# Kernel optimization log

Hardware: AMD Instinct MI355X
Metric: run time of the kernel (lower is better)

Reference implementation:

```python
import jax, jax.numpy as jnp
import numpy as np

B, S, D, CH = 4, 2048, 1024, 64
MEM_LR, MEM_MOM, MEM_DECAY = 0.1, 0.9, 0.01
EPS = 1.1920929e-07  # torch RMSNorm default eps (float32 finfo eps)


def setup_inputs() -> dict:
    key = jax.random.key(0)
    ks = jax.random.split(key, 20)
    rn = lambda i, shape, s: jax.random.normal(ks[i], shape, dtype=jnp.float32) * s
    inp = {
        "x": jax.random.normal(ks[0], (B, S, D), dtype=jnp.float32),
        # archetypal metric M = I + small perturbation (near-identity, as in ArchetypalProjection)
        "Mmet": jnp.eye(D, dtype=jnp.float32)[None, :, :] + rn(1, (B, D, D), 0.02),
        # projections (bias-free, xavier-ish scale)
        "Wk": rn(2, (D, D), 0.02), "Wv": rn(3, (D, D), 0.02),
        "Wq": rn(4, (D, D), 0.02), "Wo": rn(5, (D, D), 0.02),
        # gate Linears (with bias) for decay / lr / momentum
        "Wgd": rn(6, (D, D), 0.02), "bgd": rn(7, (D,), 0.02),
        "Wgl": rn(8, (D, D), 0.02), "bgl": rn(9, (D,), 0.02),
        "Wgm": rn(10, (D, D), 0.02), "bgm": rn(11, (D,), 0.02),
        # RMSNorm gains
        "g_store": jnp.ones((D,), dtype=jnp.float32),
        "g_retr": jnp.ones((D,), dtype=jnp.float32),
        # memory MLP initial weights (depth=2, std=0.02)
        "W0": rn(12, (D, D), 0.02), "W1": rn(13, (D, D), 0.02),
    }
    return inp


def rmsnorm(x, g):
    return x * jax.lax.rsqrt(jnp.mean(x * x, axis=-1, keepdims=True) + EPS) * g


def l2norm(x):
    n = jnp.linalg.norm(x, axis=-1, keepdims=True)
    return x / jnp.maximum(n, 1e-12)


def mem_fwd(h, W0, W1):
    # 2-layer bias-free MLP with SiLU between layers (MemoryMLP, depth=2)
    return jax.nn.silu(h @ W0.T) @ W1.T


def forward(x, Mmet, Wk, Wv, Wq, Wo, Wgd, bgd, Wgl, bgl, Wgm, bgm, g_store, g_retr, W0, W1):
    Bs, Ss, Ds = x.shape
    pad = (-Ss) % CH
    xp = jnp.pad(x, ((0, 0), (0, pad), (0, 0))) if pad else x
    N = xp.shape[1] // CH

    # data-dependent per-chunk gates from chunk means -> batch-averaged scalars [N]
    cm = xp.reshape(Bs, N, CH, Ds).mean(axis=2)            # [B,N,D]
    alpha = jax.nn.sigmoid(cm @ Wgd.T + bgd).mean(-1).mean(0) * MEM_DECAY  # [N]
    theta = jax.nn.sigmoid(cm @ Wgl.T + bgl).mean(-1).mean(0) * MEM_LR     # [N]
    eta = jax.nn.sigmoid(cm @ Wgm.T + bgm).mean(-1).mean(0) * MEM_MOM      # [N]

    # store path: RMSNorm -> curved-space keys via archetypal metric
    xs = rmsnorm(xp, g_store)
    k = l2norm(jax.nn.silu(jnp.einsum('bsd,bde->bse', xs, Mmet) @ Wk.T))
    v = jax.nn.silu(xs @ Wv.T)
    # retrieve path
    q = l2norm(jax.nn.silu(rmsnorm(xp, g_retr) @ Wq.T))

    to_chunks = lambda t: t.reshape(Bs, N, CH, Ds).transpose(1, 0, 2, 3)  # [N,B,C,D]
    kc, vc, qc = to_chunks(k), to_chunks(v), to_chunks(q)

    def assoc_loss(params, kk, vv):
        return jnp.mean((mem_fwd(kk, *params) - vv) ** 2)

    grad_fn = jax.grad(assoc_loss)

    def step(carry, inp):
        W0c, W1c, S0, S1 = carry
        qt, kt, vt, a, th, et = inp
        r = mem_fwd(qt, W0c, W1c)                 # retrieve BEFORE update (causal)
        g0, g1 = grad_fn((W0c, W1c), kt, vt)      # surprise gradient
        S0n = et * S0 - th * g0                   # Eq. 14
        S1n = et * S1 - th * g1
        W0n = (1.0 - a) * W0c + S0n               # Eq. 13
        W1n = (1.0 - a) * W1c + S1n
        return (W0n, W1n, S0n, S1n), r

    init = (W0, W1, jnp.zeros_like(W0), jnp.zeros_like(W1))
    _, ret = jax.lax.scan(step, init, (qc, kc, vc, alpha, theta, eta))  # ret: [N,B,C,D]
    out = ret.transpose(1, 0, 2, 3).reshape(Bs, N * CH, Ds)[:, :Ss, :] @ Wo.T
    return out


def reference(x, Mmet, Wk, Wv, Wq, Wo, Wgd, bgd, Wgl, bgl, Wgm, bgm, g_store, g_retr, W0, W1):
    return forward(x, Mmet, Wk, Wv, Wq, Wo, Wgd, bgd, Wgl, bgl, Wgm, bgm, g_store, g_retr, W0, W1)
```

## Files before the change

### kernel.cpp

```cpp
#include <hip/hip_runtime.h>
#include <math.h>

static constexpr int B_ = 4, S_ = 2048, D_ = 1024, CH_ = 64, N_ = 32;
static constexpr float EPS_ = 1.1920929e-07f;
static constexpr float C2_  = 2.0f / 262144.0f;
static constexpr int GRID_ = 128;

typedef __attribute__((ext_vector_type(8))) short bf16x8;
typedef __attribute__((ext_vector_type(4))) short bf16x4;
typedef __attribute__((ext_vector_type(4))) float f32x4;

__device__ __forceinline__ float sigf(float x)  { return 1.f/(1.f+expf(-x)); }
__device__ __forceinline__ float siluf(float x) { return x/(1.f+expf(-x)); }
__device__ __forceinline__ float silugrad(float x){
  float s = 1.f/(1.f+expf(-x));
  return s*(1.f + x*(1.f-s));
}
__device__ __forceinline__ short f2b(float f){
  union{float f;unsigned u;}c; c.f=f;
  unsigned u=c.u;
  return (short)((u + 0x7fffu + ((u>>16)&1u)) >> 16);
}
__device__ __forceinline__ float b2f(short h){
  union{unsigned u;float f;}c; c.u=((unsigned)(unsigned short)h)<<16; return c.f;
}

template<int LPS>
__device__ __forceinline__ void wait_vm(int c){
  if (c <= 0)      asm volatile("s_waitcnt vmcnt(0)" ::: "memory");
  else if (c == 1) asm volatile("s_waitcnt vmcnt(%0)" :: "i"(LPS)   : "memory");
  else             asm volatile("s_waitcnt vmcnt(%0)" :: "i"(2*LPS) : "memory");
}

template<int MT, int NT, int DEPTH>
__device__ __forceinline__ void score(
    const short* __restrict__ A, const short* __restrict__ Bm,
    int K, int lda, int ldb, int bm0, int bn0, short* stg,
    f32x4 (&acc)[MT/32][NT/32])
{
  constexpr int MF = MT/32, NF = NT/32;
  constexpr int ACH = MT*8, BCH = NT*8, T = 256;
  constexpr int BUF = (MT+NT)*64;
  constexpr int LPS = (ACH+BCH)/T;
  const int tid = threadIdx.x, lane = tid & 63, w = tid >> 6;
  const int wm = w>>1, wn = w&1, lrow = lane & 15, lk8 = lane >> 4;

  #pragma unroll
  for (int i=0;i<MF;++i)
    #pragma unroll
    for (int j=0;j<NF;++j) acc[i][j] = (f32x4){0.f,0.f,0.f,0.f};

  auto stage = [&](int s){
    short* la = stg + (s & (DEPTH-1))*BUF;
    short* lb = la + MT*64;
    const int k0 = s*64;
    #pragma unroll
    for (int i=tid; i<ACH; i+=T){
      int row = i>>3, sc = (i&7) ^ (row&7);
      const short* src = A + (size_t)(bm0+row)*lda + k0 + (sc<<3);
      __builtin_amdgcn_global_load_lds(
        (const __attribute__((address_space(1))) void*)src,
        (__attribute__((address_space(3))) void*)(la + i*8), 16, 0, 0);
    }
    #pragma unroll
    for (int i=tid; i<BCH; i+=T){
      int row = i>>3, sc = (i&7) ^ (row&7);
      const short* src = Bm + (size_t)(bn0+row)*ldb + k0 + (sc<<3);
      __builtin_amdgcn_global_load_lds(
        (const __attribute__((address_space(1))) void*)src,
        (__attribute__((address_space(3))) void*)(lb + i*8), 16, 0, 0);
    }
  };

  const int nk = K >> 6;
  for (int s=0; s<DEPTH-1 && s<nk; ++s) stage(s);
  for (int ks=0; ks<nk; ++ks){
    int C = nk - ks; if (C > DEPTH-1) C = DEPTH-1;
    wait_vm<LPS>(C-1);
    __builtin_amdgcn_s_barrier();
    __builtin_amdgcn_sched_barrier(0);
    if (ks + DEPTH-1 < nk) stage(ks + DEPTH-1);
    short* la = stg + (ks & (DEPTH-1))*BUF;
    short* lb = la + MT*64;
    #pragma unroll
    for (int kk=0; kk<2; ++kk){
      bf16x8 af[MF], bfr[NF];
      #pragma unroll
      for (int mi=0;mi<MF;++mi){
        int row = wm*(MT/2) + mi*16 + lrow;
        int ch = row*8 + ((kk*4+lk8) ^ (row&7));
        af[mi] = *(const bf16x8*)(la + ch*8);
      }
      #pragma unroll
      for (int ni=0;ni<NF;++ni){
        int row = wn*(NT/2) + ni*16 + lrow;
        int ch = row*8 + ((kk*4+lk8) ^ (row&7));
        bfr[ni] = *(const bf16x8*)(lb + ch*8);
      }
      #pragma unroll
      for (int mi=0;mi<MF;++mi)
        #pragma unroll
        for (int ni=0;ni<NF;++ni)
          acc[mi][ni] = __builtin_amdgcn_mfma_f32_16x16x32_bf16(af[mi], bfr[ni], acc[mi][ni], 0,0,0);
    }
  }
}

template<int WMW, int WNW, int DEPTH, class Epi>
__device__ __forceinline__ void gemm_core(
    const short* __restrict__ A, const short* __restrict__ Bm,
    int K, int lda, int ldb, int bm0, int bn0, short* lds, Epi epi)
{
  constexpr int BK = 64, CPR = 8;
  constexpr int BMR = WMW*64, BNR = WNW*64, T = WMW*WNW*64;
  constexpr int ACH = BMR*CPR, BCH = BNR*CPR;
  constexpr int BUF = (BMR+BNR)*BK;
  constexpr int LPS = (ACH+BCH)/T;
  const int tid = threadIdx.x, lane = tid & 63, w = tid >> 6;
  const int wm = w / WNW, wn = w % WNW, lrow = lane & 15, lk8 = lane >> 4;

  f32x4 acc[4][4];
  #pragma unroll
  for (int i=0;i<4;++i)
    #pragma unroll
    for (int j=0;j<4;++j) acc[i][j] = (f32x4){0.f,0.f,0.f,0.f};

  auto stage = [&](int s){
    short* la = lds + (s & (DEPTH-1))*BUF;
    short* lb = la + BMR*BK;
    const int k0 = s*BK;
    #pragma unroll
    for (int i=tid; i<ACH; i+=T){
      int row = i>>3, sc = (i&7) ^ (row&7);
      const short* src = A + (size_t)(bm0+row)*lda + k0 + (sc<<3);
      __builtin_amdgcn_global_load_lds(
        (const __attribute__((address_space(1))) void*)src,
        (__attribute__((address_space(3))) void*)(la + i*8), 16, 0, 0);
    }
    #pragma unroll
    for (int i=tid; i<BCH; i+=T){
      int row = i>>3, sc = (i&7) ^ (row&7);
      const short* src = Bm + (size_t)(bn0+row)*ldb + k0 + (sc<<3);
      __builtin_amdgcn_global_load_lds(
        (const __attribute__((address_space(1))) void*)src,
        (__attribute__((address_space(3))) void*)(lb + i*8), 16, 0, 0);
    }
  };

  const int nk = K >> 6;
  for (int s=0; s<DEPTH-1 && s<nk; ++s) stage(s);
  for (int ks=0; ks<nk; ++ks){
    int C = nk - ks; if (C > DEPTH-1) C = DEPTH-1;
    wait_vm<LPS>(C-1);
    __builtin_amdgcn_s_barrier();
    __builtin_amdgcn_sched_barrier(0);
    if (ks + DEPTH-1 < nk) stage(ks + DEPTH-1);
    short* la = lds + (ks & (DEPTH-1))*BUF;
    short* lb = la + BMR*BK;
    #pragma unroll
    for (int kk=0; kk<2; ++kk){
      bf16x8 af[4], bfr[4];
      #pragma unroll
      for (int mi=0;mi<4;++mi){
        int row = wm*64 + mi*16 + lrow;
        int ch = row*8 + ((kk*4+lk8) ^ (row&7));
        af[mi] = *(const bf16x8*)(la + ch*8);
      }
      #pragma unroll
      for (int ni=0;ni<4;++ni){
        int row = wn*64 + ni*16 + lrow;
        int ch = row*8 + ((kk*4+lk8) ^ (row&7));
        bfr[ni] = *(const bf16x8*)(lb + ch*8);
      }
      #pragma unroll
      for (int mi=0;mi<4;++mi)
        #pragma unroll
        for (int ni=0;ni<4;++ni)
          acc[mi][ni] = __builtin_amdgcn_mfma_f32_16x16x32_bf16(af[mi], bfr[ni], acc[mi][ni], 0,0,0);
    }
  }
  #pragma unroll
  for (int mi=0;mi<4;++mi)
    #pragma unroll
    for (int ni=0;ni<4;++ni)
      epi(bm0 + wm*64 + mi*16 + lk8*4, bn0 + wn*64 + ni*16 + lrow, acc[mi][ni]);
}

struct EpiOut { float* C;
  __device__ void operator()(int r0,int c,f32x4 q) const {
    #pragma unroll
    for (int j=0;j<4;++j) C[(size_t)(r0+j)*D_+c]=q[j]; } };

struct EpiStoreBf { short* C;
  __device__ void operator()(int r0,int c,f32x4 q) const {
    #pragma unroll
    for (int j=0;j<4;++j) C[(size_t)(r0+j)*D_+c]=f2b(q[j]); } };

struct EpiBiasSig { float* C; const float* bias;
  __device__ void operator()(int r0,int c,f32x4 q) const {
    #pragma unroll
    for (int j=0;j<4;++j) C[(size_t)(r0+j)*D_+c] = sigf(q[j] + bias[c]); } };

struct EpiScat { short* dst; int part;
  __device__ void operator()(int r0,int c,f32x4 q) const {
    #pragma unroll
    for (int j=0;j<4;++j){
      int r = r0+j;
      int b = r >> 11, s = r & 2047, t = s >> 6, ch = s & 63;
      short sv = f2b(siluf(q[j]));
      if (part < 0) dst[((size_t)t*256 +             b*64 + ch)*D_ + c] = sv;
      else          dst[((size_t)t*512 + part*256 + b*64 + ch)*D_ + c] = sv;
    } } };

template<int WMW, int WNW, class Epi>
__global__ __launch_bounds__(WMW*WNW*64)
void mgemm(const short* __restrict__ A, const short* __restrict__ Bm,
           int K, int lda, int ldb, Epi epi){
  __shared__ __align__(16) short lds[2*(WMW+WNW)*64*64];
  gemm_core<WMW,WNW,2>(A, Bm, K, lda, ldb, blockIdx.y*WMW*64, blockIdx.x*WNW*64, lds, epi);
}

__device__ __forceinline__ void gsync(int* flags, int ep, bool do_rel, bool do_acq){
  asm volatile("s_waitcnt vmcnt(0) lgkmcnt(0)" ::: "memory");
  __syncthreads();
  const int bid = blockIdx.x, tid = threadIdx.x;
  int* rel = flags + 2048;
  if (tid == 0){
    if (do_rel) __builtin_amdgcn_fence(__ATOMIC_RELEASE, "agent");
    __hip_atomic_store(&flags[bid*16], ep, __ATOMIC_RELAXED, __HIP_MEMORY_SCOPE_SYSTEM);
  }
  if (bid == 0){
    if (tid < 64){
      for(;;){
        int a = __hip_atomic_load(&flags[tid*16],      __ATOMIC_RELAXED, __HIP_MEMORY_SCOPE_SYSTEM);
        int b = __hip_atomic_load(&flags[(tid+64)*16], __ATOMIC_RELAXED, __HIP_MEMORY_SCOPE_SYSTEM);
        if (__all(a >= ep && b >= ep)) break;
        __builtin_amdgcn_s_sleep(1);
      }
    }
    __syncthreads();
    if (tid == 0)
      __hip_atomic_store(rel, ep, __ATOMIC_RELAXED, __HIP_MEMORY_SCOPE_SYSTEM);
  }
  if (tid == 0){
    if (bid != 0)
      while (__hip_atomic_load(rel, __ATOMIC_RELAXED, __HIP_MEMORY_SCOPE_SYSTEM) < ep)
        __builtin_amdgcn_s_sleep(1);
    if (do_acq) __builtin_amdgcn_fence(__ATOMIC_ACQUIRE, "agent");
  }
  __syncthreads();
}

__global__ __launch_bounds__(256)
void scan_coop(const short* __restrict__ qk, const short* __restrict__ vbuf,
               const short* __restrict__ ktT, const float* __restrict__ gates,
               short* __restrict__ preout, short* __restrict__ sgT,
               short* __restrict__ abuf, short* __restrict__ akT,
               short* __restrict__ dpred, short* __restrict__ dpredT, short* __restrict__ dh1T,
               const float* __restrict__ W0f, const float* __restrict__ W1f,
               short* __restrict__ W0b, short* __restrict__ W1b,
               short* __restrict__ W1bT0, short* __restrict__ W1bT1,
               int* __restrict__ bar)
{
  __shared__ __align__(16) float wM[128*132];
  __shared__ __align__(16) short stg[32768];
  const int bid = blockIdx.x;
  const int tid = threadIdx.x, lane = tid & 63, w = tid >> 6;
  const int wm = w>>1, wn = w&1, lrow = lane & 15, lk8 = lane >> 4;
  int ep = 0;

  const bool ownW1 = bid < 64;
  const int ob = ownW1 ? bid : bid - 64;
  const int obm = (ob>>3)<<7, obn = (ob&7)<<7;
  const float* Wsrc = ownW1 ? W1f : W0f;
  for (int i=tid; i<4096; i+=256){
    int cl = i>>5, r4 = (i&31)<<2;
    f32x4 v = *(const f32x4*)&Wsrc[(size_t)(obn+cl)*D_ + obm + r4];
    *(f32x4*)&wM[cl*132 + r4] = v;
  }
  f32x4 sReg[4][4];
  #pragma unroll
  for (int i=0;i<4;++i)
    #pragma unroll
    for (int j=0;j<4;++j) sReg[i][j] = (f32x4){0.f,0.f,0.f,0.f};
  __syncthreads();

  const int pbm0 = (bid>>4)<<6, pbn0 = (bid&15)<<6;

  for (int t=0; t<N_; ++t){
    const short* qkt = qk + (size_t)t*512*D_;
    const float al = gates[t], th = gates[N_+t], et = gates[2*N_+t];
    short* W1Tcur = (t&1) ? W1bT1 : W1bT0;
    short* W1Tnxt = (t&1) ? W1bT0 : W1bT1;

    {
      f32x4 acc[2][2];
      score<64,64,4>(qkt, W0b, 1024, 1024, 1024, pbm0, pbn0, stg, acc);
      #pragma unroll
      for (int mi=0;mi<2;++mi)
        #pragma unroll
        for (int ni=0;ni<2;++ni){
          int r0 = pbm0 + wm*32 + mi*16 + lk8*4;
          int c  = pbn0 + wn*32 + ni*16 + lrow;
          f32x4 q = acc[mi][ni];
          bf16x4 a4, g4;
          #pragma unroll
          for (int j=0;j<4;++j){
            a4[j] = f2b(siluf(q[j]));
            g4[j] = f2b(silugrad(q[j]));
            abuf[(size_t)(r0+j)*D_+c] = a4[j];
          }
          if (r0 >= 256){ int rr = r0-256;
            *(bf16x4*)&akT[(size_t)c*256+rr] = a4;
            *(bf16x4*)&sgT[(size_t)c*256+rr] = g4; }
        }
    }
    gsync(bar, ++ep, true, true);

    {
      const short* vt = vbuf + (size_t)t*256*D_;
      f32x4 acc[2][2];
      score<64,64,4>(abuf, W1b, 1024, 1024, 1024, pbm0, pbn0, stg, acc);
      #pragma unroll
      for (int mi=0;mi<2;++mi)
        #pragma unroll
        for (int ni=0;ni<2;++ni){
          int r0 = pbm0 + wm*32 + mi*16 + lk8*4;
          int c  = pbn0 + wn*32 + ni*16 + lrow;
          f32x4 q = acc[mi][ni];
          if (r0 < 256){
            #pragma unroll
            for (int j=0;j<4;++j){ int r=r0+j, b=r>>6, ch=r&63;
              preout[((size_t)b*S_ + t*CH_ + ch)*D_ + c] = f2b(q[j]); }
          } else { int rr = r0-256;
            bf16x4 d4;
            #pragma unroll
            for (int j=0;j<4;++j){
              float dv = C2_*(q[j] - b2f(vt[(size_t)(rr+j)*D_+c]));
              d4[j] = f2b(dv);
              dpred[(size_t)(rr+j)*D_+c] = d4[j];
            }
            *(bf16x4*)&dpredT[(size_t)c*256+rr] = d4; }
        }
    }
    if (t == N_-1) break;
    gsync(bar, ++ep, true, true);

    if (ownW1){
      f32x4 acc[4][4];
      score<128,128,2>(akT, dpredT, 256, 256, 256, obm, obn, stg, acc);
      #pragma unroll
      for (int mi=0;mi<4;++mi)
        #pragma unroll
        for (int ni=0;ni<4;++ni){
          int rl = wm*64 + mi*16 + lk8*4;
          int cl = wn*64 + ni*16 + lrow;
          f32x4 w4 = *(f32x4*)&wM[cl*132 + rl];
          f32x4 s4 = sReg[mi][ni];
          bf16x4 nb;
          #pragma unroll
          for (int j=0;j<4;++j){
            float sv = et*s4[j] - th*acc[mi][ni][j];
            s4[j] = sv;
            float wv = (1.f-al)*w4[j] + sv;
            w4[j] = wv; nb[j] = f2b(wv);
          }
          sReg[mi][ni] = s4;
          *(f32x4*)&wM[cl*132 + rl] = w4;
          int r0 = obm + rl, c = obn + cl;
          *(bf16x4*)&W1b[(size_t)c*D_ + r0] = nb;
          #pragma unroll
          for (int j=0;j<4;++j) W1Tnxt[(size_t)(r0+j)*D_ + c] = nb[j];
        }
    } else {
      int b = bid - 64;
      int bm0 = (b&15)<<6, bn0 = (b>>4)<<6;
      f32x4 acc[2][2];
      score<64,64,4>(W1Tcur, dpred, 1024, 1024, 1024, bm0, bn0, stg, acc);
      #pragma unroll
      for (int mi=0;mi<2;++mi)
        #pragma unroll
        for (int ni=0;ni<2;++ni){
          int r0 = bm0 + wm*32 + mi*16 + lk8*4;
          int c  = bn0 + wn*32 + ni*16 + lrow;
          #pragma unroll
          for (int j=0;j<4;++j){
            size_t i = (size_t)(r0+j)*256 + c;
            dh1T[i] = f2b(acc[mi][ni][j] * b2f(sgT[i]));
          }
        }
    }
    gsync(bar, ++ep, !ownW1, !ownW1);

    if (!ownW1){
      f32x4 acc[4][4];
      score<128,128,2>(ktT + (size_t)t*D_*256, dh1T, 256, 256, 256, obm, obn, stg, acc);
      #pragma unroll
      for (int mi=0;mi<4;++mi)
        #pragma unroll
        for (int ni=0;ni<4;++ni){
          int rl = wm*64 + mi*16 + lk8*4;
          int cl = wn*64 + ni*16 + lrow;
          f32x4 w4 = *(f32x4*)&wM[cl*132 + rl];
          f32x4 s4 = sReg[mi][ni];
          bf16x4 nb;
          #pragma unroll
          for (int j=0;j<4;++j){
            float sv = et*s4[j] - th*acc[mi][ni][j];
            s4[j] = sv;
            float wv = (1.f-al)*w4[j] + sv;
            w4[j] = wv; nb[j] = f2b(wv);
          }
          sReg[mi][ni] = s4;
          *(f32x4*)&wM[cl*132 + rl] = w4;
          int r0 = obm + rl, c = obn + cl;
          *(bf16x4*)&W0b[(size_t)c*D_ + r0] = nb;
        }
    }
    gsync(bar, ++ep, true, true);
  }
}

__device__ __forceinline__ float block_sum(float v){
  #pragma unroll
  for (int o=32;o>0;o>>=1) v += __shfl_down(v,o,64);
  __shared__ float sm4[4];
  int lane = threadIdx.x & 63, w = threadIdx.x >> 6;
  if (lane==0) sm4[w]=v;
  __syncthreads();
  float r = sm4[0]+sm4[1]+sm4[2]+sm4[3];
  __syncthreads();
  return r;
}

__global__ void conv_k(const float* __restrict__ s, short* __restrict__ d, int n4){
  int i = blockIdx.x*256 + threadIdx.x;
  if (i >= n4) return;
  float4 v = ((const float4*)s)[i];
  bf16x4 o = { f2b(v.x), f2b(v.y), f2b(v.z), f2b(v.w) };
  ((bf16x4*)d)[i] = o;
}

__global__ __launch_bounds__(256)
void transpose_bf_k(const short* __restrict__ in, short* __restrict__ out,
                    int R, int C, size_t ibs, size_t obs){
  __shared__ short t[64][68];
  const short* ip = in + blockIdx.z*ibs;
  short* op = out + blockIdx.z*obs;
  int r0 = blockIdx.y*64, c0 = blockIdx.x*64;
  for (int i=threadIdx.x; i<1024; i+=256){
    int r = i>>4, c4 = (i&15)*4;
    *(bf16x4*)&t[r][c4] = *(const bf16x4*)&ip[(size_t)(r0+r)*C + c0+c4];
  }
  __syncthreads();
  for (int i=threadIdx.x; i<1024; i+=256){
    int c = i>>4, r4 = (i&15)*4;
    bf16x4 v = { t[r4+0][c], t[r4+1][c], t[r4+2][c], t[r4+3][c] };
    *(bf16x4*)&op[(size_t)(c0+c)*R + r0+r4] = v;
  }
}

__global__ __launch_bounds__(256)
void transpose_f2b_k(const float* __restrict__ in, short* __restrict__ out,
                     int R, int C, size_t ibs, size_t obs){
  __shared__ short t[64][68];
  const float* ip = in + blockIdx.z*ibs;
  short* op = out + blockIdx.z*obs;
  int r0 = blockIdx.y*64, c0 = blockIdx.x*64;
  for (int i=threadIdx.x; i<1024; i+=256){
    int r = i>>4, c4 = (i&15)*4;
    float4 v = *(const float4*)&ip[(size_t)(r0+r)*C + c0+c4];
    t[r][c4+0]=f2b(v.x); t[r][c4+1]=f2b(v.y); t[r][c4+2]=f2b(v.z); t[r][c4+3]=f2b(v.w);
  }
  __syncthreads();
  for (int i=threadIdx.x; i<1024; i+=256){
    int c = i>>4, r4 = (i&15)*4;
    bf16x4 v = { t[r4+0][c], t[r4+1][c], t[r4+2][c], t[r4+3][c] };
    *(bf16x4*)&op[(size_t)(c0+c)*R + r0+r4] = v;
  }
}

__global__ void chunk_mean_k(const float* __restrict__ x, short* __restrict__ cm){
  int idx = blockIdx.x*256 + threadIdx.x;
  int d  = idx & (D_-1);
  int bn = idx >> 10;
  int b = bn >> 5, n = bn & 31;
  const float* p = x + ((size_t)b*S_ + n*CH_)*D_ + d;
  float s = 0.f;
  for (int ch=0; ch<CH_; ++ch) s += p[(size_t)ch*D_];
  cm[idx] = f2b(s * (1.f/CH_));
}

__global__ void gate_reduce_k(const float* __restrict__ Z, float* __restrict__ outp, float scale){
  int n = blockIdx.x;
  float s = 0.f;
  for (int b=0;b<B_;++b){
    const float* row = Z + (size_t)(b*N_+n)*D_;
    for (int j=threadIdx.x; j<D_; j+=256) s += row[j];
  }
  float tot = block_sum(s);
  if (threadIdx.x==0) outp[n] = scale * tot / (float)(B_*D_);
}

__global__ void rmsnorm2_k(const float* __restrict__ x, const float* __restrict__ gs,
                           const float* __restrict__ gr, short* __restrict__ xs, short* __restrict__ xr){
  size_t row = blockIdx.x;
  const float* xp = x + row*D_;
  float s = 0.f;
  for (int j=threadIdx.x;j<D_;j+=256){ float v=xp[j]; s+=v*v; }
  float tot = block_sum(s);
  float rinv = rsqrtf(tot/(float)D_ + EPS_);
  for (int j=threadIdx.x;j<D_;j+=256){
    float v = xp[j]*rinv;
    xs[row*D_+j] = f2b(v*gs[j]);
    xr[row*D_+j] = f2b(v*gr[j]);
  }
}

__global__ void l2norm_b(short* __restrict__ qk){
  size_t row = blockIdx.x;
  short* p = qk + row*D_;
  float s = 0.f;
  for (int j=threadIdx.x;j<D_;j+=256){ float v=b2f(p[j]); s+=v*v; }
  float tot = block_sum(s);
  float inv = 1.f / fmaxf(sqrtf(tot), 1e-12f);
  for (int j=threadIdx.x;j<D_;j+=256) p[j] = f2b(b2f(p[j])*inv);
}

__global__ void init_state_k(const float* __restrict__ W0, const float* __restrict__ W1,
                             short* __restrict__ W0b, short* __restrict__ W1b,
                             int* __restrict__ bar){
  size_t i = (size_t)blockIdx.x*256 + threadIdx.x;
  W0b[i]=f2b(W0[i]); W1b[i]=f2b(W1[i]);
  if (i < 4096) bar[i] = 0;
}

extern "C" void kernel_launch(void* const* d_in, const int* in_sizes, int n_in,
                              void* d_out, int out_size, void* d_ws, size_t ws_size,
                              hipStream_t stream) {
  (void)in_sizes; (void)n_in; (void)out_size;
  const float* x    = (const float*)d_in[0];
  const float* Mmet = (const float*)d_in[1];
  const float* Wk   = (const float*)d_in[2];
  const float* Wv   = (const float*)d_in[3];
  const float* Wq   = (const float*)d_in[4];
  const float* Wo   = (const float*)d_in[5];
  const float* Wgd  = (const float*)d_in[6];
  const float* bgd  = (const float*)d_in[7];
  const float* Wgl  = (const float*)d_in[8];
  const float* bgl  = (const float*)d_in[9];
  const float* Wgm  = (const float*)d_in[10];
  const float* bgm  = (const float*)d_in[11];
  const float* g_store = (const float*)d_in[12];
  const float* g_retr  = (const float*)d_in[13];
  const float* W0   = (const float*)d_in[14];
  const float* W1   = (const float*)d_in[15];
  float* out = (float*)d_out;

  if (ws_size < 145000000ull) return;
  short* qk    = (short*)d_ws;
  short* vbuf  = qk    + 16777216;
  short* xs    = vbuf  + 8388608;
  short* xr    = xs    + 8388608;
  short* t1    = xr    + 8388608;
  short* cm    = t1    + 8388608;
  short* Wkb   = cm    + 131072;
  short* Wvb   = Wkb   + 1048576;
  short* Wqb   = Wvb   + 1048576;
  short* Wob   = Wqb   + 1048576;
  short* Wgdb  = Wob   + 1048576;
  short* Wglb  = Wgdb  + 1048576;
  short* Wgmb  = Wglb  + 1048576;
  short* MmetT = Wgmb  + 1048576;
  short* W0b   = MmetT + 4194304;
  short* W1b   = W0b   + 1048576;
  short* W1bT0 = W1b   + 1048576;
  short* W1bT1 = W1bT0 + 1048576;
  short* abuf  = W1bT1 + 1048576;
  short* akT   = abuf  + 524288;
  short* sgT   = akT   + 262144;
  short* dpred = sgT   + 262144;
  short* dpredT= dpred + 262144;
  short* dh1T  = dpredT+ 262144;
  float* Zg    = (float*)(dh1T + 262144);
  float* gates = Zg    + 131072;
  int*   bar   = (int*)(gates + 128);
  short* ktT   = xr;
  short* preout= t1;

  conv_k<<<1024,256,0,stream>>>(Wk,  Wkb,  262144);
  conv_k<<<1024,256,0,stream>>>(Wv,  Wvb,  262144);
  conv_k<<<1024,256,0,stream>>>(Wq,  Wqb,  262144);
  conv_k<<<1024,256,0,stream>>>(Wo,  Wob,  262144);
  conv_k<<<1024,256,0,stream>>>(Wgd, Wgdb, 262144);
  conv_k<<<1024,256,0,stream>>>(Wgl, Wglb, 262144);
  conv_k<<<1024,256,0,stream>>>(Wgm, Wgmb, 262144);
  transpose_f2b_k<<<dim3(16,16,4),256,0,stream>>>(Mmet, MmetT, 1024, 1024, 1048576, 1048576);
  init_state_k<<<4096,256,0,stream>>>(W0, W1, W0b, W1b, bar);
  transpose_bf_k<<<dim3(16,16,1),256,0,stream>>>(W1b, W1bT0, 1024, 1024, 0, 0);

  chunk_mean_k<<<512,256,0,stream>>>(x, cm);
  {
    dim3 g(8,1);
    mgemm<2,2,EpiBiasSig><<<g,256,0,stream>>>(cm, Wgdb, 1024,1024,1024, EpiBiasSig{Zg, bgd});
    gate_reduce_k<<<N_,256,0,stream>>>(Zg, gates + 0,    0.01f);
    mgemm<2,2,EpiBiasSig><<<g,256,0,stream>>>(cm, Wglb, 1024,1024,1024, EpiBiasSig{Zg, bgl});
    gate_reduce_k<<<N_,256,0,stream>>>(Zg, gates + N_,   0.1f);
    mgemm<2,2,EpiBiasSig><<<g,256,0,stream>>>(cm, Wgmb, 1024,1024,1024, EpiBiasSig{Zg, bgm});
    gate_reduce_k<<<N_,256,0,stream>>>(Zg, gates + 2*N_, 0.9f);
  }
  rmsnorm2_k<<<B_*S_,256,0,stream>>>(x, g_store, g_retr, xs, xr);
  for (int b=0;b<B_;++b)
    mgemm<2,2,EpiStoreBf><<<dim3(8,16),256,0,stream>>>(
      xs + (size_t)b*S_*D_, MmetT + (size_t)b*D_*D_, 1024,1024,1024,
      EpiStoreBf{t1 + (size_t)b*S_*D_});
  {
    dim3 g(8,64);
    mgemm<2,2,EpiScat><<<g,256,0,stream>>>(t1, Wkb, 1024,1024,1024, EpiScat{qk, 1});
    mgemm<2,2,EpiScat><<<g,256,0,stream>>>(xs, Wvb, 1024,1024,1024, EpiScat{vbuf,-1});
    mgemm<2,2,EpiScat><<<g,256,0,stream>>>(xr, Wqb, 1024,1024,1024, EpiScat{qk, 0});
  }
  l2norm_b<<<N_*512,256,0,stream>>>(qk);
  transpose_bf_k<<<dim3(16,4,32),256,0,stream>>>(qk + 256*1024, ktT, 256, 1024,
                                                 (size_t)512*1024, (size_t)1024*256);

  scan_coop<<<GRID_,256,0,stream>>>(qk, vbuf, ktT, gates, preout, sgT, abuf, akT,
                                    dpred, dpredT, dh1T, W0, W1,
                                    W0b, W1b, W1bT0, W1bT1, bar);

  mgemm<2,2,EpiOut><<<dim3(8,64),256,0,stream>>>(preout, Wob, 1024,1024,1024, EpiOut{out});
}
```

Measured before the change: 2.213 ms.

## Double scan workgroup to 512 threads and flatten grid barrier

The cooperative scan kernel moves from 4 to 8 waves per workgroup, with a 2x4 wave layout in the tile GEMM helper, so each wave owns half as many output fragments and the per-thread accumulator and momentum register arrays shrink. The grid barrier drops the two-level scheme where block 0 gathers all flags and publishes a release word. Each block now polls all 128 flags directly. This aims to hide more latency per CU and remove one hop from each of the per-step global syncs, at the cost of more polling traffic on the flag lines and less reuse of LDS fragments per wave.

Result: slower. 2.278 ms (+2.9%).

```diff
diff --git a/kernel.cpp b/kernel.cpp
--- a/kernel.cpp
+++ b/kernel.cpp
@@ -33,17 +33,17 @@
 }
 
 template<int MT, int NT, int DEPTH>
-__device__ __forceinline__ void score(
+__device__ __forceinline__ void score8(
     const short* __restrict__ A, const short* __restrict__ Bm,
     int K, int lda, int ldb, int bm0, int bn0, short* stg,
-    f32x4 (&acc)[MT/32][NT/32])
+    f32x4 (&acc)[MT/32][NT/64])
 {
-  constexpr int MF = MT/32, NF = NT/32;
-  constexpr int ACH = MT*8, BCH = NT*8, T = 256;
+  constexpr int MF = MT/32, NF = NT/64;
+  constexpr int ACH = MT*8, BCH = NT*8, T = 512;
   constexpr int BUF = (MT+NT)*64;
   constexpr int LPS = (ACH+BCH)/T;
   const int tid = threadIdx.x, lane = tid & 63, w = tid >> 6;
-  const int wm = w>>1, wn = w&1, lrow = lane & 15, lk8 = lane >> 4;
+  const int wm = w>>2, wn = w&3, lrow = lane & 15, lk8 = lane >> 4;
 
   #pragma unroll
   for (int i=0;i<MF;++i)
@@ -93,7 +93,7 @@
       }
       #pragma unroll
       for (int ni=0;ni<NF;++ni){
-        int row = wn*(NT/2) + ni*16 + lrow;
+        int row = wn*(NT/4) + ni*16 + lrow;
         int ch = row*8 + ((kk*4+lk8) ^ (row&7));
         bfr[ni] = *(const bf16x8*)(lb + ch*8);
       }
@@ -223,35 +223,24 @@
 __device__ __forceinline__ void gsync(int* flags, int ep, bool do_rel, bool do_acq){
   asm volatile("s_waitcnt vmcnt(0) lgkmcnt(0)" ::: "memory");
   __syncthreads();
-  const int bid = blockIdx.x, tid = threadIdx.x;
-  int* rel = flags + 2048;
+  const int tid = threadIdx.x;
   if (tid == 0){
     if (do_rel) __builtin_amdgcn_fence(__ATOMIC_RELEASE, "agent");
-    __hip_atomic_store(&flags[bid*16], ep, __ATOMIC_RELAXED, __HIP_MEMORY_SCOPE_SYSTEM);
-  }
-  if (bid == 0){
-    if (tid < 64){
-      for(;;){
-        int a = __hip_atomic_load(&flags[tid*16],      __ATOMIC_RELAXED, __HIP_MEMORY_SCOPE_SYSTEM);
-        int b = __hip_atomic_load(&flags[(tid+64)*16], __ATOMIC_RELAXED, __HIP_MEMORY_SCOPE_SYSTEM);
-        if (__all(a >= ep && b >= ep)) break;
-        __builtin_amdgcn_s_sleep(1);
-      }
-    }
-    __syncthreads();
-    if (tid == 0)
-      __hip_atomic_store(rel, ep, __ATOMIC_RELAXED, __HIP_MEMORY_SCOPE_SYSTEM);
-  }
-  if (tid == 0){
-    if (bid != 0)
-      while (__hip_atomic_load(rel, __ATOMIC_RELAXED, __HIP_MEMORY_SCOPE_SYSTEM) < ep)
-        __builtin_amdgcn_s_sleep(1);
-    if (do_acq) __builtin_amdgcn_fence(__ATOMIC_ACQUIRE, "agent");
-  }
+    __hip_atomic_store(&flags[blockIdx.x*16], ep, __ATOMIC_RELAXED, __HIP_MEMORY_SCOPE_SYSTEM);
+  }
+  if (tid < 64){
+    for(;;){
+      int a = __hip_atomic_load(&flags[tid*16],      __ATOMIC_RELAXED, __HIP_MEMORY_SCOPE_SYSTEM);
+      int b = __hip_atomic_load(&flags[(tid+64)*16], __ATOMIC_RELAXED, __HIP_MEMORY_SCOPE_SYSTEM);
+      if (__all(a >= ep && b >= ep)) break;
+      __builtin_amdgcn_s_sleep(1);
+    }
+  }
+  if (tid == 0 && do_acq) __builtin_amdgcn_fence(__ATOMIC_ACQUIRE, "agent");
   __syncthreads();
 }
 
-__global__ __launch_bounds__(256)
+__global__ __launch_bounds__(512)
 void scan_coop(const short* __restrict__ qk, const short* __restrict__ vbuf,
                const short* __restrict__ ktT, const float* __restrict__ gates,
                short* __restrict__ preout, short* __restrict__ sgT,
@@ -266,23 +255,23 @@
   __shared__ __align__(16) short stg[32768];
   const int bid = blockIdx.x;
   const int tid = threadIdx.x, lane = tid & 63, w = tid >> 6;
-  const int wm = w>>1, wn = w&1, lrow = lane & 15, lk8 = lane >> 4;
+  const int wm = w>>2, wn = w&3, lrow = lane & 15, lk8 = lane >> 4;
   int ep = 0;
 
   const bool ownW1 = bid < 64;
   const int ob = ownW1 ? bid : bid - 64;
   const int obm = (ob>>3)<<7, obn = (ob&7)<<7;
   const float* Wsrc = ownW1 ? W1f : W0f;
-  for (int i=tid; i<4096; i+=256){
+  for (int i=tid; i<4096; i+=512){
     int cl = i>>5, r4 = (i&31)<<2;
     f32x4 v = *(const f32x4*)&Wsrc[(size_t)(obn+cl)*D_ + obm + r4];
     *(f32x4*)&wM[cl*132 + r4] = v;
   }
-  f32x4 sReg[4][4];
+  f32x4 sReg[4][2];
   #pragma unroll
   for (int i=0;i<4;++i)
     #pragma unroll
-    for (int j=0;j<4;++j) sReg[i][j] = (f32x4){0.f,0.f,0.f,0.f};
+    for (int j=0;j<2;++j) sReg[i][j] = (f32x4){0.f,0.f,0.f,0.f};
   __syncthreads();
 
   const int pbm0 = (bid>>4)<<6, pbn0 = (bid&15)<<6;
@@ -294,67 +283,63 @@
     short* W1Tnxt = (t&1) ? W1bT0 : W1bT1;
 
     {
-      f32x4 acc[2][2];
-      score<64,64,4>(qkt, W0b, 1024, 1024, 1024, pbm0, pbn0, stg, acc);
-      #pragma unroll
-      for (int mi=0;mi<2;++mi)
+      f32x4 acc[2][1];
+      score8<64,64,4>(qkt, W0b, 1024, 1024, 1024, pbm0, pbn0, stg, acc);
+      #pragma unroll
+      for (int mi=0;mi<2;++mi){
+        int r0 = pbm0 + wm*32 + mi*16 + lk8*4;
+        int c  = pbn0 + wn*16 + lrow;
+        f32x4 q = acc[mi][0];
+        bf16x4 a4, g4;
+        #pragma unroll
+        for (int j=0;j<4;++j){
+          a4[j] = f2b(siluf(q[j]));
+          g4[j] = f2b(silugrad(q[j]));
+          abuf[(size_t)(r0+j)*D_+c] = a4[j];
+        }
+        if (r0 >= 256){ int rr = r0-256;
+          *(bf16x4*)&akT[(size_t)c*256+rr] = a4;
+          *(bf16x4*)&sgT[(size_t)c*256+rr] = g4; }
+      }
+    }
+    gsync(bar, ++ep, true, true);
+
+    {
+      const short* vt = vbuf + (size_t)t*256*D_;
+      f32x4 acc[2][1];
+      score8<64,64,4>(abuf, W1b, 1024, 1024, 1024, pbm0, pbn0, stg, acc);
+      #pragma unroll
+      for (int mi=0;mi<2;++mi){
+        int r0 = pbm0 + wm*32 + mi*16 + lk8*4;
+        int c  = pbn0 + wn*16 + lrow;
+        f32x4 q = acc[mi][0];
+        if (r0 < 256){
+          #pragma unroll
+          for (int j=0;j<4;++j){ int r=r0+j, b=r>>6, ch=r&63;
+            preout[((size_t)b*S_ + t*CH_ + ch)*D_ + c] = f2b(q[j]); }
+        } else { int rr = r0-256;
+          bf16x4 d4;
+          #pragma unroll
+          for (int j=0;j<4;++j){
+            float dv = C2_*(q[j] - b2f(vt[(size_t)(rr+j)*D_+c]));
+            d4[j] = f2b(dv);
+            dpred[(size_t)(rr+j)*D_+c] = d4[j];
+          }
+          *(bf16x4*)&dpredT[(size_t)c*256+rr] = d4; }
+      }
+    }
+    if (t == N_-1) break;
+    gsync(bar, ++ep, true, true);
+
+    if (ownW1){
+      f32x4 acc[4][2];
+      score8<128,128,2>(akT, dpredT, 256, 256, 256, obm, obn, stg, acc);
+      #pragma unroll
+      for (int mi=0;mi<4;++mi)
         #pragma unroll
         for (int ni=0;ni<2;++ni){
-          int r0 = pbm0 + wm*32 + mi*16 + lk8*4;
-          int c  = pbn0 + wn*32 + ni*16 + lrow;
-          f32x4 q = acc[mi][ni];
-          bf16x4 a4, g4;
-          #pragma unroll
-          for (int j=0;j<4;++j){
-            a4[j] = f2b(siluf(q[j]));
-            g4[j] = f2b(silugrad(q[j]));
-            abuf[(size_t)(r0+j)*D_+c] = a4[j];
-          }
-          if (r0 >= 256){ int rr = r0-256;
-            *(bf16x4*)&akT[(size_t)c*256+rr] = a4;
-            *(bf16x4*)&sgT[(size_t)c*256+rr] = g4; }
-        }
-    }
-    gsync(bar, ++ep, true, true);
-
-    {
-      const short* vt = vbuf + (size_t)t*256*D_;
-      f32x4 acc[2][2];
-      score<64,64,4>(abuf, W1b, 1024, 1024, 1024, pbm0, pbn0, stg, acc);
-      #pragma unroll
-      for (int mi=0;mi<2;++mi)
-        #pragma unroll
-        for (int ni=0;ni<2;++ni){
-          int r0 = pbm0 + wm*32 + mi*16 + lk8*4;
-          int c  = pbn0 + wn*32 + ni*16 + lrow;
-          f32x4 q = acc[mi][ni];
-          if (r0 < 256){
-            #pragma unroll
-            for (int j=0;j<4;++j){ int r=r0+j, b=r>>6, ch=r&63;
-              preout[((size_t)b*S_ + t*CH_ + ch)*D_ + c] = f2b(q[j]); }
-          } else { int rr = r0-256;
-            bf16x4 d4;
-            #pragma unroll
-            for (int j=0;j<4;++j){
-              float dv = C2_*(q[j] - b2f(vt[(size_t)(rr+j)*D_+c]));
-              d4[j] = f2b(dv);
-              dpred[(size_t)(rr+j)*D_+c] = d4[j];
-            }
-            *(bf16x4*)&dpredT[(size_t)c*256+rr] = d4; }
-        }
-    }
-    if (t == N_-1) break;
-    gsync(bar, ++ep, true, true);
-
-    if (ownW1){
-      f32x4 acc[4][4];
-      score<128,128,2>(akT, dpredT, 256, 256, 256, obm, obn, stg, acc);
-      #pragma unroll
-      for (int mi=0;mi<4;++mi)
-        #pragma unroll
-        for (int ni=0;ni<4;++ni){
           int rl = wm*64 + mi*16 + lk8*4;
-          int cl = wn*64 + ni*16 + lrow;
+          int cl = wn*32 + ni*16 + lrow;
           f32x4 w4 = *(f32x4*)&wM[cl*132 + rl];
           f32x4 s4 = sReg[mi][ni];
           bf16x4 nb;
@@ -375,32 +360,30 @@
     } else {
       int b = bid - 64;
       int bm0 = (b&15)<<6, bn0 = (b>>4)<<6;
-      f32x4 acc[2][2];
-      score<64,64,4>(W1Tcur, dpred, 1024, 1024, 1024, bm0, bn0, stg, acc);
-      #pragma unroll
-      for (int mi=0;mi<2;++mi)
+      f32x4 acc[2][1];
+      score8<64,64,4>(W1Tcur, dpred, 1024, 1024, 1024, bm0, bn0, stg, acc);
+      #pragma unroll
+      for (int mi=0;mi<2;++mi){
+        int r0 = bm0 + wm*32 + mi*16 + lk8*4;
+        int c  = bn0 + wn*16 + lrow;
+        #pragma unroll
+        for (int j=0;j<4;++j){
+          size_t i = (size_t)(r0+j)*256 + c;
+          dh1T[i] = f2b(acc[mi][0][j] * b2f(sgT[i]));
+        }
+      }
+    }
+    gsync(bar, ++ep, !ownW1, !ownW1);
+
+    if (!ownW1){
+      f32x4 acc[4][2];
+      score8<128,128,2>(ktT + (size_t)t*D_*256, dh1T, 256, 256, 256, obm, obn, stg, acc);
+      #pragma unroll
+      for (int mi=0;mi<4;++mi)
         #pragma unroll
         for (int ni=0;ni<2;++ni){
-          int r0 = bm0 + wm*32 + mi*16 + lk8*4;
-          int c  = bn0 + wn*32 + ni*16 + lrow;
-          #pragma unroll
-          for (int j=0;j<4;++j){
-            size_t i = (size_t)(r0+j)*256 + c;
-            dh1T[i] = f2b(acc[mi][ni][j] * b2f(sgT[i]));
-          }
-        }
-    }
-    gsync(bar, ++ep, !ownW1, !ownW1);
-
-    if (!ownW1){
-      f32x4 acc[4][4];
-      score<128,128,2>(ktT + (size_t)t*D_*256, dh1T, 256, 256, 256, obm, obn, stg, acc);
-      #pragma unroll
-      for (int mi=0;mi<4;++mi)
-        #pragma unroll
-        for (int ni=0;ni<4;++ni){
           int rl = wm*64 + mi*16 + lk8*4;
-          int cl = wn*64 + ni*16 + lrow;
+          int cl = wn*32 + ni*16 + lrow;
           f32x4 w4 = *(f32x4*)&wM[cl*132 + rl];
           f32x4 s4 = sReg[mi][ni];
           bf16x4 nb;
@@ -624,7 +607,7 @@
   transpose_bf_k<<<dim3(16,4,32),256,0,stream>>>(qk + 256*1024, ktT, 256, 1024,
                                                  (size_t)512*1024, (size_t)1024*256);
 
-  scan_coop<<<GRID_,256,0,stream>>>(qk, vbuf, ktT, gates, preout, sgT, abuf, akT,
+  scan_coop<<<GRID_,512,0,stream>>>(qk, vbuf, ktT, gates, preout, sgT, abuf, akT,
                                     dpred, dpredT, dh1T, W0, W1,
                                     W0b, W1b, W1bT0, W1bT1, bar);
 
```

## Compute dh1 slice locally per W0-owner block to drop a grid barrier

Applied to the files above, without the earlier changes.

Each W0-owning block now computes the 128 hidden rows of dh1 it needs (W1^T·dpred times silu-grad) into a private scratch slice. It then runs the ktT·dh1 gradient GEMM on that slice right away instead of waiting on a grid-wide sync for a shared dh1T buffer. This removes one cooperative barrier per scan step. In exchange each block does more GEMM work (two 128x128 tiles instead of one 64x64), and the workspace grows to hold the per-block slices.

After: 2.946 ms. 1.33x slower.

```diff
diff --git a/kernel.cpp b/kernel.cpp
--- a/kernel.cpp
+++ b/kernel.cpp
@@ -256,7 +256,7 @@
                const short* __restrict__ ktT, const float* __restrict__ gates,
                short* __restrict__ preout, short* __restrict__ sgT,
                short* __restrict__ abuf, short* __restrict__ akT,
-               short* __restrict__ dpred, short* __restrict__ dpredT, short* __restrict__ dh1T,
+               short* __restrict__ dpred, short* __restrict__ dpredT, short* __restrict__ dh1p,
                const float* __restrict__ W0f, const float* __restrict__ W1f,
                short* __restrict__ W0b, short* __restrict__ W1b,
                short* __restrict__ W1bT0, short* __restrict__ W1bT1,
@@ -286,6 +286,7 @@
   __syncthreads();
 
   const int pbm0 = (bid>>4)<<6, pbn0 = (bid&15)<<6;
+  short* myd = dh1p + (size_t)(ownW1 ? 0 : (bid-64))*128*256;
 
   for (int t=0; t<N_; ++t){
     const short* qkt = qk + (size_t)t*512*D_;
@@ -373,51 +374,51 @@
           for (int j=0;j<4;++j) W1Tnxt[(size_t)(r0+j)*D_ + c] = nb[j];
         }
     } else {
-      int b = bid - 64;
-      int bm0 = (b&15)<<6, bn0 = (b>>4)<<6;
-      f32x4 acc[2][2];
-      score<64,64,4>(W1Tcur, dpred, 1024, 1024, 1024, bm0, bn0, stg, acc);
-      #pragma unroll
-      for (int mi=0;mi<2;++mi)
+      for (int rh=0; rh<2; ++rh){
+        f32x4 acc[4][4];
+        score<128,128,2>(W1Tcur, dpred, 1024, 1024, 1024, obn, rh*128, stg, acc);
         #pragma unroll
-        for (int ni=0;ni<2;++ni){
-          int r0 = bm0 + wm*32 + mi*16 + lk8*4;
-          int c  = bn0 + wn*32 + ni*16 + lrow;
+        for (int mi=0;mi<4;++mi)
           #pragma unroll
-          for (int j=0;j<4;++j){
-            size_t i = (size_t)(r0+j)*256 + c;
-            dh1T[i] = f2b(acc[mi][ni][j] * b2f(sgT[i]));
+          for (int ni=0;ni<4;++ni){
+            int hg = obn + wm*64 + mi*16 + lk8*4;
+            int rg = rh*128 + wn*64 + ni*16 + lrow;
+            #pragma unroll
+            for (int j=0;j<4;++j){
+              float dv = acc[mi][ni][j] * b2f(sgT[(size_t)(hg+j)*256 + rg]);
+              myd[(size_t)(hg - obn + j)*256 + rg] = f2b(dv);
+            }
           }
-        }
-    }
-    gsync(bar, ++ep, !ownW1, !ownW1);
-
-    if (!ownW1){
-      f32x4 acc[4][4];
-      score<128,128,2>(ktT + (size_t)t*D_*256, dh1T, 256, 256, 256, obm, obn, stg, acc);
-      #pragma unroll
-      for (int mi=0;mi<4;++mi)
+      }
+      asm volatile("s_waitcnt vmcnt(0)" ::: "memory");
+      __syncthreads();
+      {
+        f32x4 acc[4][4];
+        score<128,128,2>(ktT + (size_t)t*D_*256, myd, 256, 256, 256, obm, 0, stg, acc);
         #pragma unroll
-        for (int ni=0;ni<4;++ni){
-          int rl = wm*64 + mi*16 + lk8*4;
-          int cl = wn*64 + ni*16 + lrow;
-          f32x4 w4 = *(f32x4*)&wM[cl*132 + rl];
-          f32x4 s4 = sReg[mi][ni];
-          bf16x4 nb;
+        for (int mi=0;mi<4;++mi)
           #pragma unroll
-          for (int j=0;j<4;++j){
-            float sv = et*s4[j] - th*acc[mi][ni][j];
-            s4[j] = sv;
-            float wv = (1.f-al)*w4[j] + sv;
-            w4[j] = wv; nb[j] = f2b(wv);
+          for (int ni=0;ni<4;++ni){
+            int rl = wm*64 + mi*16 + lk8*4;
+            int cl = wn*64 + ni*16 + lrow;
+            f32x4 w4 = *(f32x4*)&wM[cl*132 + rl];
+            f32x4 s4 = sReg[mi][ni];
+            bf16x4 nb;
+            #pragma unroll
+            for (int j=0;j<4;++j){
+              float sv = et*s4[j] - th*acc[mi][ni][j];
+              s4[j] = sv;
+              float wv = (1.f-al)*w4[j] + sv;
+              w4[j] = wv; nb[j] = f2b(wv);
+            }
+            sReg[mi][ni] = s4;
+            *(f32x4*)&wM[cl*132 + rl] = w4;
+            int r0 = obm + rl, c = obn + cl;
+            *(bf16x4*)&W0b[(size_t)c*D_ + r0] = nb;
           }
-          sReg[mi][ni] = s4;
-          *(f32x4*)&wM[cl*132 + rl] = w4;
-          int r0 = obm + rl, c = obn + cl;
-          *(bf16x4*)&W0b[(size_t)c*D_ + r0] = nb;
-        }
-    }
-    gsync(bar, ++ep, true, true);
+      }
+    }
+    gsync(bar, ++ep, !ownW1, true);
   }
 }
 
@@ -557,7 +558,7 @@
   const float* W1   = (const float*)d_in[15];
   float* out = (float*)d_out;
 
-  if (ws_size < 145000000ull) return;
+  if (ws_size < 152000000ull) return;
   short* qk    = (short*)d_ws;
   short* vbuf  = qk    + 16777216;
   short* xs    = vbuf  + 8388608;
@@ -581,10 +582,10 @@
   short* sgT   = akT   + 262144;
   short* dpred = sgT   + 262144;
   short* dpredT= dpred + 262144;
-  short* dh1T  = dpredT+ 262144;
-  float* Zg    = (float*)(dh1T + 262144);
+  float* Zg    = (float*)(dpredT + 262144);
   float* gates = Zg    + 131072;
   int*   bar   = (int*)(gates + 128);
+  short* dh1p  = (short*)(bar + 4096);
   short* ktT   = xr;
   short* preout= t1;
 
@@ -625,7 +626,7 @@
                                                  (size_t)512*1024, (size_t)1024*256);
 
   scan_coop<<<GRID_,256,0,stream>>>(qk, vbuf, ktT, gates, preout, sgT, abuf, akT,
-                                    dpred, dpredT, dh1T, W0, W1,
+                                    dpred, dpredT, dh1p, W0, W1,
                                     W0b, W1b, W1bT0, W1bT1, bar);
 
   mgemm<2,2,EpiOut><<<dim3(8,64),256,0,stream>>>(preout, Wob, 1024,1024,1024, EpiOut{out});
```

## Keep fp32 master weights in registers and deepen GEMM prefetch pipeline

Applied to the files above, without the earlier changes.

Moves the per-block fp32 master weight tile from shared memory into registers (wReg), which frees LDS. The freed space doubles the staging buffer so every score GEMM can use a deeper multi-stage prefetch (DEPTH 4→8 for 64x64 tiles, 2→4 for 128x128 tiles), and wait_vm is extended to handle the larger in-flight counts. The aim is to hide global-load latency inside the serial scan's GEMMs. In exchange, register pressure rises by 64 floats per thread, which could cause spills or lower occupancy.

Result: slower. 3.610 ms (+63.1%).

```diff
diff --git a/kernel.cpp b/kernel.cpp
--- a/kernel.cpp
+++ b/kernel.cpp
@@ -27,9 +27,15 @@
 
 template<int LPS>
 __device__ __forceinline__ void wait_vm(int c){
-  if (c <= 0)      asm volatile("s_waitcnt vmcnt(0)" ::: "memory");
-  else if (c == 1) asm volatile("s_waitcnt vmcnt(%0)" :: "i"(LPS)   : "memory");
-  else             asm volatile("s_waitcnt vmcnt(%0)" :: "i"(2*LPS) : "memory");
+  switch(c){
+    case 0: asm volatile("s_waitcnt vmcnt(0)" ::: "memory"); break;
+    case 1: asm volatile("s_waitcnt vmcnt(%0)" :: "i"(1*LPS) : "memory"); break;
+    case 2: asm volatile("s_waitcnt vmcnt(%0)" :: "i"(2*LPS) : "memory"); break;
+    case 3: asm volatile("s_waitcnt vmcnt(%0)" :: "i"(3*LPS) : "memory"); break;
+    case 4: asm volatile("s_waitcnt vmcnt(%0)" :: "i"(4*LPS) : "memory"); break;
+    case 5: asm volatile("s_waitcnt vmcnt(%0)" :: "i"(5*LPS) : "memory"); break;
+    default: asm volatile("s_waitcnt vmcnt(%0)" :: "i"(6*LPS) : "memory"); break;
+  }
 }
 
 template<int MT, int NT, int DEPTH>
@@ -262,8 +268,7 @@
                short* __restrict__ W1bT0, short* __restrict__ W1bT1,
                int* __restrict__ bar)
 {
-  __shared__ __align__(16) float wM[128*132];
-  __shared__ __align__(16) short stg[32768];
+  __shared__ __align__(16) short stg[65536];
   const int bid = blockIdx.x;
   const int tid = threadIdx.x, lane = tid & 63, w = tid >> 6;
   const int wm = w>>1, wn = w&1, lrow = lane & 15, lk8 = lane >> 4;
@@ -273,17 +278,17 @@
   const int ob = ownW1 ? bid : bid - 64;
   const int obm = (ob>>3)<<7, obn = (ob&7)<<7;
   const float* Wsrc = ownW1 ? W1f : W0f;
-  for (int i=tid; i<4096; i+=256){
-    int cl = i>>5, r4 = (i&31)<<2;
-    f32x4 v = *(const f32x4*)&Wsrc[(size_t)(obn+cl)*D_ + obm + r4];
-    *(f32x4*)&wM[cl*132 + r4] = v;
-  }
-  f32x4 sReg[4][4];
+
+  f32x4 wReg[4][4], sReg[4][4];
   #pragma unroll
-  for (int i=0;i<4;++i)
-    #pragma unroll
-    for (int j=0;j<4;++j) sReg[i][j] = (f32x4){0.f,0.f,0.f,0.f};
-  __syncthreads();
+  for (int mi=0;mi<4;++mi)
+    #pragma unroll
+    for (int ni=0;ni<4;++ni){
+      int rl = wm*64 + mi*16 + lk8*4;
+      int cl = wn*64 + ni*16 + lrow;
+      wReg[mi][ni] = *(const f32x4*)&Wsrc[(size_t)(obn+cl)*D_ + obm + rl];
+      sReg[mi][ni] = (f32x4){0.f,0.f,0.f,0.f};
+    }
 
   const int pbm0 = (bid>>4)<<6, pbn0 = (bid&15)<<6;
 
@@ -295,7 +300,7 @@
 
     {
       f32x4 acc[2][2];
-      score<64,64,4>(qkt, W0b, 1024, 1024, 1024, pbm0, pbn0, stg, acc);
+      score<64,64,8>(qkt, W0b, 1024, 1024, 1024, pbm0, pbn0, stg, acc);
       #pragma unroll
       for (int mi=0;mi<2;++mi)
         #pragma unroll
@@ -320,7 +325,7 @@
     {
       const short* vt = vbuf + (size_t)t*256*D_;
       f32x4 acc[2][2];
-      score<64,64,4>(abuf, W1b, 1024, 1024, 1024, pbm0, pbn0, stg, acc);
+      score<64,64,8>(abuf, W1b, 1024, 1024, 1024, pbm0, pbn0, stg, acc);
       #pragma unroll
       for (int mi=0;mi<2;++mi)
         #pragma unroll
@@ -348,14 +353,14 @@
 
     if (ownW1){
       f32x4 acc[4][4];
-      score<128,128,2>(akT, dpredT, 256, 256, 256, obm, obn, stg, acc);
+      score<128,128,4>(akT, dpredT, 256, 256, 256, obm, obn, stg, acc);
       #pragma unroll
       for (int mi=0;mi<4;++mi)
         #pragma unroll
         for (int ni=0;ni<4;++ni){
           int rl = wm*64 + mi*16 + lk8*4;
           int cl = wn*64 + ni*16 + lrow;
-          f32x4 w4 = *(f32x4*)&wM[cl*132 + rl];
+          f32x4 w4 = wReg[mi][ni];
           f32x4 s4 = sReg[mi][ni];
           bf16x4 nb;
           #pragma unroll
@@ -366,7 +371,7 @@
             w4[j] = wv; nb[j] = f2b(wv);
           }
           sReg[mi][ni] = s4;
-          *(f32x4*)&wM[cl*132 + rl] = w4;
+          wReg[mi][ni] = w4;
           int r0 = obm + rl, c = obn + cl;
           *(bf16x4*)&W1b[(size_t)c*D_ + r0] = nb;
           #pragma unroll
@@ -376,7 +381,7 @@
       int b = bid - 64;
       int bm0 = (b&15)<<6, bn0 = (b>>4)<<6;
       f32x4 acc[2][2];
-      score<64,64,4>(W1Tcur, dpred, 1024, 1024, 1024, bm0, bn0, stg, acc);
+      score<64,64,8>(W1Tcur, dpred, 1024, 1024, 1024, bm0, bn0, stg, acc);
       #pragma unroll
       for (int mi=0;mi<2;++mi)
         #pragma unroll
@@ -394,14 +399,14 @@
 
     if (!ownW1){
       f32x4 acc[4][4];
-      score<128,128,2>(ktT + (size_t)t*D_*256, dh1T, 256, 256, 256, obm, obn, stg, acc);
+      score<128,128,4>(ktT + (size_t)t*D_*256, dh1T, 256, 256, 256, obm, obn, stg, acc);
       #pragma unroll
       for (int mi=0;mi<4;++mi)
         #pragma unroll
         for (int ni=0;ni<4;++ni){
           int rl = wm*64 + mi*16 + lk8*4;
           int cl = wn*64 + ni*16 + lrow;
-          f32x4 w4 = *(f32x4*)&wM[cl*132 + rl];
+          f32x4 w4 = wReg[mi][ni];
           f32x4 s4 = sReg[mi][ni];
           bf16x4 nb;
           #pragma unroll
@@ -412,7 +417,7 @@
             w4[j] = wv; nb[j] = f2b(wv);
           }
           sReg[mi][ni] = s4;
-          *(f32x4*)&wM[cl*132 + rl] = w4;
+          wReg[mi][ni] = w4;
           int r0 = obm + rl, c = obn + cl;
           *(bf16x4*)&W0b[(size_t)c*D_ + r0] = nb;
         }
```
